# Kernel optimization log

Hardware: AMD Instinct MI355X
Metric: run time of the kernel (lower is better)

Reference implementation:

```python
import jax, jax.numpy as jnp
import numpy as np

N = 1048576          # num_features (columns)
EMBED = 128          # embed_dim
ATTR = EMBED // 5    # 25, per-attribute embedding dim for 4 tables
REM = EMBED - 4 * ATTR  # 28, trading-pair embedding dim
N_LEVELS, N_TYPES, N_FEATS, N_EXCH, N_PAIRS = 50, 2, 2, 3, 20


def setup_inputs() -> dict:
    key = jax.random.key(0)
    ks = jax.random.split(key, 12)
    return {
        "level_tab": jax.random.normal(ks[0], (N_LEVELS, ATTR), jnp.float32),
        "type_tab": jax.random.normal(ks[1], (N_TYPES, ATTR), jnp.float32),
        "feature_tab": jax.random.normal(ks[2], (N_FEATS, ATTR), jnp.float32),
        "exchange_tab": jax.random.normal(ks[3], (N_EXCH, ATTR), jnp.float32),
        "pair_tab": jax.random.normal(ks[4], (N_PAIRS, REM), jnp.float32),
        "W": jax.random.normal(ks[5], (EMBED, EMBED), jnp.float32) / np.sqrt(EMBED),
        "b": jax.random.normal(ks[6], (EMBED,), jnp.float32) * 0.01,
        "level_idx": jax.random.randint(ks[7], (N,), 0, N_LEVELS, jnp.int32),
        "type_idx": jax.random.randint(ks[8], (N,), 0, N_TYPES, jnp.int32),
        "feature_idx": jax.random.randint(ks[9], (N,), 0, N_FEATS, jnp.int32),
        "exchange_idx": jax.random.randint(ks[10], (N,), 0, N_EXCH, jnp.int32),
        "pair_idx": jax.random.randint(ks[11], (N,), 0, N_PAIRS, jnp.int32),
    }


def reference(level_tab, type_tab, feature_tab, exchange_tab, pair_tab, W, b,
              level_idx, type_idx, feature_idx, exchange_idx, pair_idx):
    # Batched gather from 5 small tables + concat -> [N, EMBED]
    combined = jnp.concatenate(
        [level_tab[level_idx],       # [N, ATTR]
         type_tab[type_idx],         # [N, ATTR]
         feature_tab[feature_idx],   # [N, ATTR]
         exchange_tab[exchange_idx], # [N, ATTR]
         pair_tab[pair_idx]],        # [N, REM]
        axis=-1)
    # Linear projection: y = x @ W^T + b (torch nn.Linear convention)
    return jnp.einsum("nf,ef->ne", combined, W) + b
```

## Files before the change

### kernel.cpp

```cpp
#include <hip/hip_runtime.h>

#define EMBED 128
#define ATTR  25
#define REM   28
#define NL 50
#define NT 2
#define NF 2
#define NE 3
#define NP 20
#define CROWS 77

__global__ __launch_bounds__(EMBED) void precompute_C(
    const float* __restrict__ level_tab,
    const float* __restrict__ type_tab,
    const float* __restrict__ feature_tab,
    const float* __restrict__ exchange_tab,
    const float* __restrict__ pair_tab,
    const float* __restrict__ W,
    const float* __restrict__ b,
    float* __restrict__ C)
{
    const int r = blockIdx.x;
    const int e = threadIdx.x;
    const float* tab;
    int off, len;
    float acc = 0.0f;
    if (r < NL)                { tab = level_tab    + r * ATTR;        off = 0;   len = ATTR; }
    else if (r < NL + NT)      { tab = type_tab     + (r - 50) * ATTR; off = 25;  len = ATTR; }
    else if (r < NL + NT + NF) { tab = feature_tab  + (r - 52) * ATTR; off = 50;  len = ATTR; }
    else if (r < 57)           { tab = exchange_tab + (r - 54) * ATTR; off = 75;  len = ATTR; acc = b[e]; }
    else                       { tab = pair_tab     + (r - 57) * REM;  off = 100; len = REM;  }

    const float* w = W + (size_t)e * EMBED + off;
    #pragma unroll 4
    for (int f = 0; f < len; ++f) acc = fmaf(w[f], tab[f], acc);
    C[r * EMBED + e] = acc;
}

__global__ __launch_bounds__(256) void gather_add(
    const int* __restrict__ li, const int* __restrict__ ti,
    const int* __restrict__ fi, const int* __restrict__ ei,
    const int* __restrict__ pi,
    const float* __restrict__ C,
    float* __restrict__ out, int N)
{
    __shared__ float4 sC[CROWS * 32];
    const float4* C4 = (const float4*)C;
    for (int i = threadIdx.x; i < CROWS * 32; i += 256) sC[i] = C4[i];
    __syncthreads();

    const int c   = threadIdx.x & 31;
    const int rib = threadIdx.x >> 5;
    const int stride = gridDim.x * 8;

    for (int n = blockIdx.x * 8 + rib; n < N; n += stride) {
        const int l = li[n];
        const int t = ti[n];
        const int f = fi[n];
        const int e = ei[n];
        const int p = pi[n];

        float4 a0 = sC[l * 32 + c];
        float4 a1 = sC[(50 + t) * 32 + c];
        float4 a2 = sC[(52 + f) * 32 + c];
        float4 a3 = sC[(54 + e) * 32 + c];
        float4 a4 = sC[(57 + p) * 32 + c];

        float4 r;
        r.x = a0.x + a1.x + a2.x + a3.x + a4.x;
        r.y = a0.y + a1.y + a2.y + a3.y + a4.y;
        r.z = a0.z + a1.z + a2.z + a3.z + a4.z;
        r.w = a0.w + a1.w + a2.w + a3.w + a4.w;

        ((float4*)(out + (size_t)n * EMBED))[c] = r;
    }
}

extern "C" void kernel_launch(void* const* d_in, const int* in_sizes, int n_in,
                              void* d_out, int out_size, void* d_ws, size_t ws_size,
                              hipStream_t stream) {
    const float* level_tab    = (const float*)d_in[0];
    const float* type_tab     = (const float*)d_in[1];
    const float* feature_tab  = (const float*)d_in[2];
    const float* exchange_tab = (const float*)d_in[3];
    const float* pair_tab     = (const float*)d_in[4];
    const float* W            = (const float*)d_in[5];
    const float* b            = (const float*)d_in[6];
    const int*   li           = (const int*)d_in[7];
    const int*   ti           = (const int*)d_in[8];
    const int*   fi           = (const int*)d_in[9];
    const int*   ei           = (const int*)d_in[10];
    const int*   pi           = (const int*)d_in[11];

    float* out = (float*)d_out;
    float* C   = (float*)d_ws;

    const int N = in_sizes[7];

    precompute_C<<<CROWS, EMBED, 0, stream>>>(
        level_tab, type_tab, feature_tab, exchange_tab, pair_tab, W, b, C);

    const int blocks = 2048;
    gather_add<<<blocks, 256, 0, stream>>>(li, ti, fi, ei, pi, C, out, N);
}
```

Baseline: 636.9 us.

## Merge type/feature/exchange tables into combined rows and process four rows per half-warp

```diff
diff --git a/kernel.cpp b/kernel.cpp
--- a/kernel.cpp
+++ b/kernel.cpp
@@ -4,11 +4,11 @@
 #define ATTR  25
 #define REM   28
 #define NL 50
-#define NT 2
-#define NF 2
-#define NE 3
+#define NTFE 12
 #define NP 20
-#define CROWS 77
+#define CROWS (NL + NTFE + NP)
+#define ROW_TFE NL
+#define ROW_PAIR (NL + NTFE)
 
 __global__ __launch_bounds__(EMBED) void precompute_C(
     const float* __restrict__ level_tab,
@@ -22,57 +22,81 @@
 {
     const int r = blockIdx.x;
     const int e = threadIdx.x;
-    const float* tab;
-    int off, len;
+    const float* w = W + (size_t)e * EMBED;
     float acc = 0.0f;
-    if (r < NL)                { tab = level_tab    + r * ATTR;        off = 0;   len = ATTR; }
-    else if (r < NL + NT)      { tab = type_tab     + (r - 50) * ATTR; off = 25;  len = ATTR; }
-    else if (r < NL + NT + NF) { tab = feature_tab  + (r - 52) * ATTR; off = 50;  len = ATTR; }
-    else if (r < 57)           { tab = exchange_tab + (r - 54) * ATTR; off = 75;  len = ATTR; acc = b[e]; }
-    else                       { tab = pair_tab     + (r - 57) * REM;  off = 100; len = REM;  }
 
-    const float* w = W + (size_t)e * EMBED + off;
-    #pragma unroll 4
-    for (int f = 0; f < len; ++f) acc = fmaf(w[f], tab[f], acc);
+    if (r < NL) {
+        const float* tab = level_tab + r * ATTR;
+        #pragma unroll
+        for (int k = 0; k < ATTR; ++k) acc = fmaf(w[k], tab[k], acc);
+    } else if (r < ROW_PAIR) {
+        const int q = r - ROW_TFE;
+        const int t = q / 6;
+        const int f = (q % 6) / 3;
+        const int ex = q % 3;
+        const float* tt = type_tab     + t  * ATTR;
+        const float* ft = feature_tab  + f  * ATTR;
+        const float* et = exchange_tab + ex * ATTR;
+        acc = b[e];
+        #pragma unroll
+        for (int k = 0; k < ATTR; ++k) {
+            acc = fmaf(w[25 + k], tt[k], acc);
+            acc = fmaf(w[50 + k], ft[k], acc);
+            acc = fmaf(w[75 + k], et[k], acc);
+        }
+    } else {
+        const float* pt = pair_tab + (r - ROW_PAIR) * REM;
+        #pragma unroll
+        for (int k = 0; k < REM; ++k) acc = fmaf(w[100 + k], pt[k], acc);
+    }
     C[r * EMBED + e] = acc;
 }
 
-__global__ __launch_bounds__(256) void gather_add(
+__global__ __launch_bounds__(512) void gather_add(
     const int* __restrict__ li, const int* __restrict__ ti,
     const int* __restrict__ fi, const int* __restrict__ ei,
     const int* __restrict__ pi,
     const float* __restrict__ C,
-    float* __restrict__ out, int N)
+    float* __restrict__ out, int N4)
 {
     __shared__ float4 sC[CROWS * 32];
     const float4* C4 = (const float4*)C;
-    for (int i = threadIdx.x; i < CROWS * 32; i += 256) sC[i] = C4[i];
+    for (int i = threadIdx.x; i < CROWS * 32; i += 512) sC[i] = C4[i];
     __syncthreads();
 
-    const int c   = threadIdx.x & 31;
-    const int rib = threadIdx.x >> 5;
-    const int stride = gridDim.x * 8;
+    const int c  = threadIdx.x & 31;
+    const int hw = threadIdx.x >> 5;
+    const int stride = gridDim.x * 16;
 
-    for (int n = blockIdx.x * 8 + rib; n < N; n += stride) {
-        const int l = li[n];
-        const int t = ti[n];
-        const int f = fi[n];
-        const int e = ei[n];
-        const int p = pi[n];
+    for (int g = blockIdx.x * 16 + hw; g < N4; g += stride) {
+        const int n0 = g * 4;
+        int4 l4 = *(const int4*)(li + n0);
+        int4 t4 = *(const int4*)(ti + n0);
+        int4 f4 = *(const int4*)(fi + n0);
+        int4 e4 = *(const int4*)(ei + n0);
+        int4 p4 = *(const int4*)(pi + n0);
 
-        float4 a0 = sC[l * 32 + c];
-        float4 a1 = sC[(50 + t) * 32 + c];
-        float4 a2 = sC[(52 + f) * 32 + c];
-        float4 a3 = sC[(54 + e) * 32 + c];
-        float4 a4 = sC[(57 + p) * 32 + c];
+        const int q0 = ROW_TFE + t4.x * 6 + f4.x * 3 + e4.x;
+        const int q1 = ROW_TFE + t4.y * 6 + f4.y * 3 + e4.y;
+        const int q2 = ROW_TFE + t4.z * 6 + f4.z * 3 + e4.z;
+        const int q3 = ROW_TFE + t4.w * 6 + f4.w * 3 + e4.w;
 
-        float4 r;
-        r.x = a0.x + a1.x + a2.x + a3.x + a4.x;
-        r.y = a0.y + a1.y + a2.y + a3.y + a4.y;
-        r.z = a0.z + a1.z + a2.z + a3.z + a4.z;
-        r.w = a0.w + a1.w + a2.w + a3.w + a4.w;
+        float4 a0 = sC[l4.x * 32 + c], b0 = sC[q0 * 32 + c], d0 = sC[(ROW_PAIR + p4.x) * 32 + c];
+        float4 a1 = sC[l4.y * 32 + c], b1 = sC[q1 * 32 + c], d1 = sC[(ROW_PAIR + p4.y) * 32 + c];
+        float4 a2 = sC[l4.z * 32 + c], b2 = sC[q2 * 32 + c], d2 = sC[(ROW_PAIR + p4.z) * 32 + c];
+        float4 a3 = sC[l4.w * 32 + c], b3 = sC[q3 * 32 + c], d3 = sC[(ROW_PAIR + p4.w) * 32 + c];
 
-        ((float4*)(out + (size_t)n * EMBED))[c] = r;
+        float4 r0, r1, r2, r3;
+        r0.x = a0.x + b0.x + d0.x; r0.y = a0.y + b0.y + d0.y; r0.z = a0.z + b0.z + d0.z; r0.w = a0.w + b0.w + d0.w;
+        r1.x = a1.x + b1.x + d1.x; r1.y = a1.y + b1.y + d1.y; r1.z = a1.z + b1.z + d1.z; r1.w = a1.w + b1.w + d1.w;
+        r2.x = a2.x + b2.x + d2.x; r2.y = a2.y + b2.y + d2.y; r2.z = a2.z + b2.z + d2.z; r2.w = a2.w + b2.w + d2.w;
+        r3.x = a3.x + b3.x + d3.x; r3.y = a3.y + b3.y + d3.y; r3.z = a3.z + b3.z + d3.z; r3.w = a3.w + b3.w + d3.w;
+
+        float4* o = (float4*)(out + (size_t)n0 * EMBED) + c;
+        o[0]  = r0;
+        o[32] = r1;
+        o[64] = r2;
+        o[96] = r3;
     }
 }
 
@@ -101,5 +125,5 @@
         level_tab, type_tab, feature_tab, exchange_tab, pair_tab, W, b, C);
 
     const int blocks = 2048;
-    gather_add<<<blocks, 256, 0, stream>>>(li, ti, fi, ei, pi, C, out, N);
+    gather_add<<<blocks, 512, 0, stream>>>(li, ti, fi, ei, pi, C, out, N / 4);
 }
```

New measurement: 592.1 us. 7.0% less time.
